# Performance work log

Hardware: AMD Instinct MI355X
Metric: run time of the kernel (lower is better)

Reference implementation:

```python
import jax, jax.numpy as jnp
import numpy as np

EPS = 1e-5

def _layernorm(x, gamma, beta):
    mu = jnp.mean(x, axis=-1, keepdims=True)
    var = jnp.mean(jnp.square(x - mu), axis=-1, keepdims=True)
    return (x - mu) * jax.lax.rsqrt(var + EPS) * gamma + beta

def setup_inputs() -> dict:
    key = jax.random.key(0)
    kx, kw = jax.random.split(key)
    N, D, BIT = 65536, 1024, 64
    X = jax.random.normal(kx, (N, D), dtype=jnp.float32)
    # xavier_uniform with gain=0.5 for weight [BIT, D]
    limit = 0.5 * np.sqrt(6.0 / (D + BIT))
    W = jax.random.uniform(kw, (BIT, D), minval=-limit, maxval=limit, dtype=jnp.float32)
    b = jnp.zeros((BIT,), dtype=jnp.float32)
    ln1_g = jnp.ones((D,), dtype=jnp.float32)
    ln1_b = jnp.zeros((D,), dtype=jnp.float32)
    ln2_g = jnp.ones((BIT,), dtype=jnp.float32)
    ln2_b = jnp.zeros((BIT,), dtype=jnp.float32)
    return {"X": X, "W": W, "b": b, "ln1_g": ln1_g, "ln1_b": ln1_b, "ln2_g": ln2_g, "ln2_b": ln2_b}

def reference(X, W, b, ln1_g, ln1_b, ln2_g, ln2_b):
    # LayerNorm -> Linear -> LayerNorm
    xn = _layernorm(X, ln1_g, ln1_b)                       # [N, D]
    logits = jnp.einsum('nd,bd->nb', xn, W) + b            # [N, BIT]
    logits = _layernorm(logits, ln2_g, ln2_b)
    # mean-center over batch, tanh, sign-binarize
    logits = logits - jnp.mean(logits, axis=0, keepdims=True)
    H = jnp.tanh(0.5 * logits)
    B = jnp.where(H >= 0.0, jnp.int8(1), jnp.int8(-1))
    return H, B
```

## Files before the change

kernel.cpp:

```cpp
#include <hip/hip_runtime.h>
#include <stdint.h>

#define N_ROWS 65536
#define D_IN   1024
#define NBIT   64
#define LN_EPS 1e-5f

typedef __attribute__((ext_vector_type(8)))  _Float16 f16x8;
typedef __attribute__((ext_vector_type(4)))  float f32x4;
typedef __attribute__((ext_vector_type(16))) float f32x16;

__device__ __forceinline__ void gload_lds16(const void* g, void* l) {
    __builtin_amdgcn_global_load_lds(
        (const __attribute__((address_space(1))) uint32_t*)g,
        (__attribute__((address_space(3))) uint32_t*)l, 16, 0, 0);
}

__device__ __forceinline__ f32x16 mfma32(f16x8 a, f16x8 b, f32x16 c) {
    return __builtin_amdgcn_mfma_f32_32x32x16_f16(a, b, c, 0, 0, 0);
}

__global__ void prep_kernel(const float* __restrict__ W, const float* __restrict__ bias,
                            const float* __restrict__ g1, const float* __restrict__ b1,
                            _Float16* __restrict__ whi, _Float16* __restrict__ wlo,
                            float* __restrict__ u, float* __restrict__ v) {
    int bit = blockIdx.x;
    int t   = threadIdx.x;
    int nt  = bit >> 5, col = bit & 31;
    float su = 0.f, sv = 0.f;
    for (int d = t; d < D_IN; d += 256) {
        float w  = W[bit * D_IN + d];
        float gw = w * g1[d];
        su += gw;
        sv += w * b1[d];
        int tg = d >> 4, c = tg >> 3, tt = tg & 7;
        int hi = (d >> 3) & 1, j = d & 7;
        int lane = col + 32 * hi;
        size_t idx = (size_t)c * 8192 + tt * 1024 + nt * 512 + lane * 8 + j;
        _Float16 h = (_Float16)gw;
        whi[idx] = h;
        wlo[idx] = (_Float16)((gw - (float)h) * 2048.0f);
    }
    __shared__ float s1[256], s2[256];
    s1[t] = su; s2[t] = sv;
    __syncthreads();
    for (int off = 128; off > 0; off >>= 1) {
        if (t < off) { s1[t] += s1[t + off]; s2[t] += s2[t + off]; }
        __syncthreads();
    }
    if (t == 0) { u[bit] = s1[0]; v[bit] = s2[0] + bias[bit]; }
}

__global__ void __launch_bounds__(256, 2) main_kernel(
        const float* __restrict__ X,
        const _Float16* __restrict__ whi, const _Float16* __restrict__ wlo,
        const float* __restrict__ u, const float* __restrict__ v,
        const float* __restrict__ g2, const float* __restrict__ b2,
        float* __restrict__ L, float* __restrict__ P) {
    __shared__ _Float16 lw[2][16384];
    int tid  = threadIdx.x;
    int wid  = tid >> 6, lane = tid & 63;
    int col  = lane & 31, hi = lane >> 5;
    int row_base = blockIdx.x * 128 + wid * 32;

    const float* xrow = X + (size_t)(row_base + col) * D_IN + hi * 8;

    const _Float16* gsrc = ((wid & 2) ? wlo : whi) + (wid & 1) * 4096 + (size_t)lane * 8;
    const int ldst = ((wid & 2) ? 8192 : 0) + (wid & 1) * 4096;

#define STAGEW(cc, buf) do {                                                  \
        const _Float16* gs_ = gsrc + (size_t)(cc) * 8192;                     \
        _Float16* ld_ = &lw[buf][ldst];                                       \
        _Pragma("unroll")                                                     \
        for (int r = 0; r < 8; ++r)                                           \
            gload_lds16(gs_ + r * 512, ld_ + r * 512);                        \
    } while (0)

    f32x16 aH0[2], aH1[2], aM[2], aLL[2];
#pragma unroll
    for (int nt = 0; nt < 2; ++nt) {
        aH0[nt] = (f32x16)(0.f); aH1[nt] = (f32x16)(0.f);
        aM[nt]  = (f32x16)(0.f); aLL[nt] = (f32x16)(0.f);
    }
    float sum = 0.f, sumsq = 0.f;

    STAGEW(0, 0);
    __syncthreads();

    for (int c = 0; c < 8; ++c) {
        if (c < 7) STAGEW(c + 1, (c + 1) & 1);
        const float* xp = xrow + c * 128;
        const _Float16* lwb = &lw[c & 1][0] + lane * 8;
#pragma unroll
        for (int t = 0; t < 8; ++t) {
            f32x4 x0 = *(const f32x4*)(xp + t * 16);
            f32x4 x1 = *(const f32x4*)(xp + t * 16 + 4);
            float xs[8] = {x0[0], x0[1], x0[2], x0[3], x1[0], x1[1], x1[2], x1[3]};
            f16x8 ahi, alo;
#pragma unroll
            for (int j = 0; j < 8; ++j) {
                float xv = xs[j];
                sum += xv;
                sumsq = fmaf(xv, xv, sumsq);
                _Float16 h = (_Float16)xv;
                ahi[j] = h;
                alo[j] = (_Float16)((xv - (float)h) * 2048.0f);
            }
            const _Float16* base = lwb + t * 1024;
#pragma unroll
            for (int nt = 0; nt < 2; ++nt) {
                f16x8 bh = *(const f16x8*)(base + nt * 512);
                f16x8 bl = *(const f16x8*)(base + nt * 512 + 8192);
                if (t & 1) aH1[nt] = mfma32(ahi, bh, aH1[nt]);
                else       aH0[nt] = mfma32(ahi, bh, aH0[nt]);
                aM[nt]  = mfma32(ahi, bl, aM[nt]);
                aM[nt]  = mfma32(alo, bh, aM[nt]);
                aLL[nt] = mfma32(alo, bl, aLL[nt]);
            }
        }
        __syncthreads();
    }

    sum   += __shfl_xor(sum, 32);
    sumsq += __shfl_xor(sumsq, 32);
    float mu   = sum * (1.f / 1024.f);
    float var  = sumsq * (1.f / 1024.f) - mu * mu;
    float rstd = rsqrtf(var + LN_EPS);

    float uv[2], vv[2], g2v[2], b2v[2];
#pragma unroll
    for (int nt = 0; nt < 2; ++nt) {
        int bitc = nt * 32 + col;
        uv[nt] = u[bitc]; vv[nt] = v[bitc]; g2v[nt] = g2[bitc]; b2v[nt] = b2[bitc];
    }

    float ps0 = 0.f, ps1 = 0.f;
#pragma unroll
    for (int reg = 0; reg < 16; ++reg) {
        int r = (reg & 3) + 8 * (reg >> 2) + 4 * hi;
        float mu_r = __shfl(mu, r);
        float rs_r = __shfl(rstd, r);
        float lg0, lg1;
        {
            float d0 = (aH0[0][reg] + aH1[0][reg])
                     + aM[0][reg] * (1.0f / 2048.0f)
                     + aLL[0][reg] * (1.0f / 4194304.0f);
            float d1 = (aH0[1][reg] + aH1[1][reg])
                     + aM[1][reg] * (1.0f / 2048.0f)
                     + aLL[1][reg] * (1.0f / 4194304.0f);
            lg0 = rs_r * d0 - rs_r * mu_r * uv[0] + vv[0];
            lg1 = rs_r * d1 - rs_r * mu_r * uv[1] + vv[1];
        }
        float s1 = lg0 + lg1;
        float s2 = lg0 * lg0 + lg1 * lg1;
#pragma unroll
        for (int m = 1; m <= 16; m <<= 1) {
            s1 += __shfl_xor(s1, m);
            s2 += __shfl_xor(s2, m);
        }
        float mean = s1 * (1.f / 64.f);
        float va   = s2 * (1.f / 64.f) - mean * mean;
        float rs2  = rsqrtf(va + LN_EPS);
        float o0 = (lg0 - mean) * rs2 * g2v[0] + b2v[0];
        float o1 = (lg1 - mean) * rs2 * g2v[1] + b2v[1];
        size_t row = (size_t)(row_base + r);
        L[row * 64 + col]      = o0;
        L[row * 64 + 32 + col] = o1;
        ps0 += o0;
        ps1 += o1;
    }

    ps0 += __shfl_xor(ps0, 32);
    ps1 += __shfl_xor(ps1, 32);
    if (hi == 0) {
        P[(size_t)col * 2048        + blockIdx.x * 4 + wid] = ps0;
        P[(size_t)(32 + col) * 2048 + blockIdx.x * 4 + wid] = ps1;
    }
#undef STAGEW
}

__global__ void reduce_kernel(const float* __restrict__ P, float* __restrict__ cm) {
    int bit = blockIdx.x, t = threadIdx.x;
    float s = 0.f;
    for (int p = t; p < 2048; p += 256) s += P[(size_t)bit * 2048 + p];
    __shared__ float sh[256];
    sh[t] = s;
    __syncthreads();
    for (int off = 128; off > 0; off >>= 1) {
        if (t < off) sh[t] += sh[t + off];
        __syncthreads();
    }
    if (t == 0) cm[bit] = sh[0] * (1.f / (float)N_ROWS);
}

__global__ void final_kernel(const float* __restrict__ L, const float* __restrict__ cm,
                             float* __restrict__ out) {
    __shared__ float cms[64];
    if (threadIdx.x < 64) cms[threadIdx.x] = cm[threadIdx.x];
    __syncthreads();
    const f32x4* L4 = (const f32x4*)L;
    f32x4* H4 = (f32x4*)out;
    f32x4* B4 = (f32x4*)(out + (size_t)N_ROWS * NBIT);
    int total = N_ROWS * NBIT / 4;
    for (int i = blockIdx.x * blockDim.x + threadIdx.x; i < total;
         i += gridDim.x * blockDim.x) {
        f32x4 x = L4[i];
        int bb = (i & 15) * 4;
        f32x4 h, bo;
#pragma unroll
        for (int j = 0; j < 4; ++j) {
            float y  = 0.5f * (x[j] - cms[bb + j]);
            float y2 = y * y;
            float poly = y * fmaf(y2, fmaf(y2, 2.f / 15.f, -1.f / 3.f), 1.f);
            float e  = __expf(2.f * y);
            float ef = 1.f - 2.f / (e + 1.f);
            float hv = (fabsf(y) < 0.5f) ? poly : ef;
            h[j]  = hv;
            bo[j] = hv >= 0.f ? 1.f : -1.f;
        }
        __builtin_nontemporal_store(h, &H4[i]);
        __builtin_nontemporal_store(bo, &B4[i]);
    }
}

extern "C" void kernel_launch(void* const* d_in, const int* in_sizes, int n_in,
                              void* d_out, int out_size, void* d_ws, size_t ws_size,
                              hipStream_t stream) {
    (void)in_sizes; (void)n_in; (void)out_size; (void)ws_size;
    const float* X  = (const float*)d_in[0];
    const float* W  = (const float*)d_in[1];
    const float* bb = (const float*)d_in[2];
    const float* g1 = (const float*)d_in[3];
    const float* b1 = (const float*)d_in[4];
    const float* g2 = (const float*)d_in[5];
    const float* b2 = (const float*)d_in[6];

    char* ws = (char*)d_ws;
    _Float16* whi = (_Float16*)ws;
    _Float16* wlo = (_Float16*)(ws + 131072);
    float* u  = (float*)(ws + 262144);
    float* v  = (float*)(ws + 266240);
    float* P  = (float*)(ws + 270336);
    float* cm = (float*)(ws + 270336 + 64 * 2048 * 4);

    float* out = (float*)d_out;
    float* L   = out + (size_t)N_ROWS * NBIT;

    prep_kernel<<<64, 256, 0, stream>>>(W, bb, g1, b1, whi, wlo, u, v);
    main_kernel<<<512, 256, 0, stream>>>(X, whi, wlo, u, v, g2, b2, L, P);
    reduce_kernel<<<64, 256, 0, stream>>>(P, cm);
    final_kernel<<<2048, 256, 0, stream>>>(L, cm, out);
}
```

Baseline: 84.39 us.

## Drop lo*lo MFMA term and use single-buffered 256-wide weight chunks

Removes the alo*blo split-precision MFMA product, which contributes at roughly 2^-22 relative scale, so each k-step issues three MFMAs per tile instead of four. The weight staging changes from double-buffered 128-wide chunks (8 iterations) to one 64KB buffer holding 256-wide chunks (4 iterations). Each next chunk is now loaded only after a barrier, with a second barrier afterwards. This trades the overlap of weight loads with compute for fewer loop iterations and a lower MFMA count, and slightly reduces accuracy.

After: 90.24 us. 6.9% more time.

```diff
diff --git a/kernel.cpp b/kernel.cpp
--- a/kernel.cpp
+++ b/kernel.cpp
@@ -33,10 +33,9 @@
         float gw = w * g1[d];
         su += gw;
         sv += w * b1[d];
-        int tg = d >> 4, c = tg >> 3, tt = tg & 7;
-        int hi = (d >> 3) & 1, j = d & 7;
-        int lane = col + 32 * hi;
-        size_t idx = (size_t)c * 8192 + tt * 1024 + nt * 512 + lane * 8 + j;
+        int c = d >> 8, tt = (d >> 4) & 15, hi8 = (d >> 3) & 1, j = d & 7;
+        int lane = col + 32 * hi8;
+        size_t idx = (size_t)c * 16384 + tt * 1024 + nt * 512 + lane * 8 + j;
         _Float16 h = (_Float16)gw;
         whi[idx] = h;
         wlo[idx] = (_Float16)((gw - (float)h) * 2048.0f);
@@ -57,7 +56,7 @@
         const float* __restrict__ u, const float* __restrict__ v,
         const float* __restrict__ g2, const float* __restrict__ b2,
         float* __restrict__ L, float* __restrict__ P) {
-    __shared__ _Float16 lw[2][16384];
+    __shared__ _Float16 lw[32768];
     int tid  = threadIdx.x;
     int wid  = tid >> 6, lane = tid & 63;
     int col  = lane & 31, hi = lane >> 5;
@@ -65,34 +64,32 @@
 
     const float* xrow = X + (size_t)(row_base + col) * D_IN + hi * 8;
 
-    const _Float16* gsrc = ((wid & 2) ? wlo : whi) + (wid & 1) * 4096 + (size_t)lane * 8;
-    const int ldst = ((wid & 2) ? 8192 : 0) + (wid & 1) * 4096;
-
-#define STAGEW(cc, buf) do {                                                  \
-        const _Float16* gs_ = gsrc + (size_t)(cc) * 8192;                     \
-        _Float16* ld_ = &lw[buf][ldst];                                       \
+    const _Float16* gsrc = ((wid & 2) ? wlo : whi) + (wid & 1) * 8192 + (size_t)lane * 8;
+    const int ldst = ((wid & 2) ? 16384 : 0) + (wid & 1) * 8192;
+
+#define STAGEW(cc) do {                                                       \
+        const _Float16* gs_ = gsrc + (size_t)(cc) * 16384;                    \
+        _Float16* ld_ = &lw[ldst];                                            \
         _Pragma("unroll")                                                     \
-        for (int r = 0; r < 8; ++r)                                           \
+        for (int r = 0; r < 16; ++r)                                          \
             gload_lds16(gs_ + r * 512, ld_ + r * 512);                        \
     } while (0)
 
-    f32x16 aH0[2], aH1[2], aM[2], aLL[2];
+    f32x16 aH0[2], aH1[2], aM[2];
 #pragma unroll
     for (int nt = 0; nt < 2; ++nt) {
-        aH0[nt] = (f32x16)(0.f); aH1[nt] = (f32x16)(0.f);
-        aM[nt]  = (f32x16)(0.f); aLL[nt] = (f32x16)(0.f);
+        aH0[nt] = (f32x16)(0.f); aH1[nt] = (f32x16)(0.f); aM[nt] = (f32x16)(0.f);
     }
     float sum = 0.f, sumsq = 0.f;
 
-    STAGEW(0, 0);
-    __syncthreads();
-
-    for (int c = 0; c < 8; ++c) {
-        if (c < 7) STAGEW(c + 1, (c + 1) & 1);
-        const float* xp = xrow + c * 128;
-        const _Float16* lwb = &lw[c & 1][0] + lane * 8;
-#pragma unroll
-        for (int t = 0; t < 8; ++t) {
+    STAGEW(0);
+    __syncthreads();
+
+    for (int c = 0; c < 4; ++c) {
+        const float* xp = xrow + c * 256;
+        const _Float16* lwb = &lw[0] + lane * 8;
+#pragma unroll
+        for (int t = 0; t < 16; ++t) {
             f32x4 x0 = *(const f32x4*)(xp + t * 16);
             f32x4 x1 = *(const f32x4*)(xp + t * 16 + 4);
             float xs[8] = {x0[0], x0[1], x0[2], x0[3], x1[0], x1[1], x1[2], x1[3]};
@@ -110,15 +107,18 @@
 #pragma unroll
             for (int nt = 0; nt < 2; ++nt) {
                 f16x8 bh = *(const f16x8*)(base + nt * 512);
-                f16x8 bl = *(const f16x8*)(base + nt * 512 + 8192);
+                f16x8 bl = *(const f16x8*)(base + nt * 512 + 16384);
                 if (t & 1) aH1[nt] = mfma32(ahi, bh, aH1[nt]);
                 else       aH0[nt] = mfma32(ahi, bh, aH0[nt]);
-                aM[nt]  = mfma32(ahi, bl, aM[nt]);
-                aM[nt]  = mfma32(alo, bh, aM[nt]);
-                aLL[nt] = mfma32(alo, bl, aLL[nt]);
+                aM[nt] = mfma32(ahi, bl, aM[nt]);
+                aM[nt] = mfma32(alo, bh, aM[nt]);
             }
         }
         __syncthreads();
+        if (c < 3) {
+            STAGEW(c + 1);
+            __syncthreads();
+        }
     }
 
     sum   += __shfl_xor(sum, 32);
@@ -140,17 +140,10 @@
         int r = (reg & 3) + 8 * (reg >> 2) + 4 * hi;
         float mu_r = __shfl(mu, r);
         float rs_r = __shfl(rstd, r);
-        float lg0, lg1;
-        {
-            float d0 = (aH0[0][reg] + aH1[0][reg])
-                     + aM[0][reg] * (1.0f / 2048.0f)
-                     + aLL[0][reg] * (1.0f / 4194304.0f);
-            float d1 = (aH0[1][reg] + aH1[1][reg])
-                     + aM[1][reg] * (1.0f / 2048.0f)
-                     + aLL[1][reg] * (1.0f / 4194304.0f);
-            lg0 = rs_r * d0 - rs_r * mu_r * uv[0] + vv[0];
-            lg1 = rs_r * d1 - rs_r * mu_r * uv[1] + vv[1];
-        }
+        float d0 = (aH0[0][reg] + aH1[0][reg]) + aM[0][reg] * (1.0f / 2048.0f);
+        float d1 = (aH0[1][reg] + aH1[1][reg]) + aM[1][reg] * (1.0f / 2048.0f);
+        float lg0 = rs_r * d0 - rs_r * mu_r * uv[0] + vv[0];
+        float lg1 = rs_r * d1 - rs_r * mu_r * uv[1] + vv[1];
         float s1 = lg0 + lg1;
         float s2 = lg0 * lg0 + lg1 * lg1;
 #pragma unroll
```

## Drop lo*lo MFMA term, prefetch next X chunk, use packed f16 conversion

Applied to the files above, without the earlier changes.

Removes the alo*bl MFMA product and its accumulator, cutting matrix work by a quarter at the cost of a tiny precision loss. The first two X vectors of the next chunk are prefetched before a manual barrier, and that barrier waits on vmcnt(4) rather than a full __syncthreads, so global loads overlap with compute. The hi/lo f16 split now uses packed round-toward-zero conversion (cvt_pkrtz), which changes rounding but keeps the residual exact. The hand-written vmcnt wait adds a correctness risk if the count of outstanding loads does not match.

Measured after the change: 81.30 us. 3.7% less time.

```diff
diff --git a/kernel.cpp b/kernel.cpp
--- a/kernel.cpp
+++ b/kernel.cpp
@@ -7,6 +7,8 @@
 #define LN_EPS 1e-5f
 
 typedef __attribute__((ext_vector_type(8)))  _Float16 f16x8;
+typedef __attribute__((ext_vector_type(4)))  _Float16 f16x4;
+typedef __attribute__((ext_vector_type(2)))  _Float16 f16x2;
 typedef __attribute__((ext_vector_type(4)))  float f32x4;
 typedef __attribute__((ext_vector_type(16))) float f32x16;
 
@@ -18,6 +20,39 @@
 
 __device__ __forceinline__ f32x16 mfma32(f16x8 a, f16x8 b, f32x16 c) {
     return __builtin_amdgcn_mfma_f32_32x32x16_f16(a, b, c, 0, 0, 0);
+}
+
+__device__ __forceinline__ f16x2 pkrtz(float a, float b) {
+    return __builtin_bit_cast(f16x2, __builtin_amdgcn_cvt_pkrtz(a, b));
+}
+
+__device__ __forceinline__ void split8(f32x4 x0, f32x4 x1,
+                                       f16x8& ahi, f16x8& alo,
+                                       float& sum, float& sumsq) {
+    float xs[8] = {x0[0], x0[1], x0[2], x0[3], x1[0], x1[1], x1[2], x1[3]};
+#pragma unroll
+    for (int j = 0; j < 8; ++j) {
+        sum += xs[j];
+        sumsq = fmaf(xs[j], xs[j], sumsq);
+    }
+    f16x2 h01 = pkrtz(xs[0], xs[1]);
+    f16x2 h23 = pkrtz(xs[2], xs[3]);
+    f16x2 h45 = pkrtz(xs[4], xs[5]);
+    f16x2 h67 = pkrtz(xs[6], xs[7]);
+    f16x2 l01 = pkrtz((xs[0] - (float)h01[0]) * 2048.f,
+                      (xs[1] - (float)h01[1]) * 2048.f);
+    f16x2 l23 = pkrtz((xs[2] - (float)h23[0]) * 2048.f,
+                      (xs[3] - (float)h23[1]) * 2048.f);
+    f16x2 l45 = pkrtz((xs[4] - (float)h45[0]) * 2048.f,
+                      (xs[5] - (float)h45[1]) * 2048.f);
+    f16x2 l67 = pkrtz((xs[6] - (float)h67[0]) * 2048.f,
+                      (xs[7] - (float)h67[1]) * 2048.f);
+    f16x4 a0 = __builtin_shufflevector(h01, h23, 0, 1, 2, 3);
+    f16x4 a1 = __builtin_shufflevector(h45, h67, 0, 1, 2, 3);
+    ahi = __builtin_shufflevector(a0, a1, 0, 1, 2, 3, 4, 5, 6, 7);
+    f16x4 b0 = __builtin_shufflevector(l01, l23, 0, 1, 2, 3);
+    f16x4 b1 = __builtin_shufflevector(l45, l67, 0, 1, 2, 3);
+    alo = __builtin_shufflevector(b0, b1, 0, 1, 2, 3, 4, 5, 6, 7);
 }
 
 __global__ void prep_kernel(const float* __restrict__ W, const float* __restrict__ bias,
@@ -34,8 +69,8 @@
         su += gw;
         sv += w * b1[d];
         int tg = d >> 4, c = tg >> 3, tt = tg & 7;
-        int hi = (d >> 3) & 1, j = d & 7;
-        int lane = col + 32 * hi;
+        int hi8 = (d >> 3) & 1, j = d & 7;
+        int lane = col + 32 * hi8;
         size_t idx = (size_t)c * 8192 + tt * 1024 + nt * 512 + lane * 8 + j;
         _Float16 h = (_Float16)gw;
         whi[idx] = h;
@@ -76,36 +111,32 @@
             gload_lds16(gs_ + r * 512, ld_ + r * 512);                        \
     } while (0)
 
-    f32x16 aH0[2], aH1[2], aM[2], aLL[2];
+#define SB0 __builtin_amdgcn_sched_barrier(0)
+
+    f32x16 aH0[2], aH1[2], aM[2];
 #pragma unroll
     for (int nt = 0; nt < 2; ++nt) {
-        aH0[nt] = (f32x16)(0.f); aH1[nt] = (f32x16)(0.f);
-        aM[nt]  = (f32x16)(0.f); aLL[nt] = (f32x16)(0.f);
+        aH0[nt] = (f32x16)(0.f); aH1[nt] = (f32x16)(0.f); aM[nt] = (f32x16)(0.f);
     }
     float sum = 0.f, sumsq = 0.f;
+    f32x4 p0, p1, p2, p3;
 
     STAGEW(0, 0);
+    p0 = *(const f32x4*)(xrow);
+    p1 = *(const f32x4*)(xrow + 4);
+    p2 = *(const f32x4*)(xrow + 16);
+    p3 = *(const f32x4*)(xrow + 20);
     __syncthreads();
 
+#pragma unroll
     for (int c = 0; c < 8; ++c) {
         if (c < 7) STAGEW(c + 1, (c + 1) & 1);
-        const float* xp = xrow + c * 128;
+        const float* xp  = xrow + c * 128;
         const _Float16* lwb = &lw[c & 1][0] + lane * 8;
-#pragma unroll
-        for (int t = 0; t < 8; ++t) {
-            f32x4 x0 = *(const f32x4*)(xp + t * 16);
-            f32x4 x1 = *(const f32x4*)(xp + t * 16 + 4);
-            float xs[8] = {x0[0], x0[1], x0[2], x0[3], x1[0], x1[1], x1[2], x1[3]};
-            f16x8 ahi, alo;
-#pragma unroll
-            for (int j = 0; j < 8; ++j) {
-                float xv = xs[j];
-                sum += xv;
-                sumsq = fmaf(xv, xv, sumsq);
-                _Float16 h = (_Float16)xv;
-                ahi[j] = h;
-                alo[j] = (_Float16)((xv - (float)h) * 2048.0f);
-            }
+        f16x8 ahi, alo;
+#pragma unroll
+        for (int t = 0; t < 2; ++t) {
+            split8(t ? p2 : p0, t ? p3 : p1, ahi, alo, sum, sumsq);
             const _Float16* base = lwb + t * 1024;
 #pragma unroll
             for (int nt = 0; nt < 2; ++nt) {
@@ -113,12 +144,36 @@
                 f16x8 bl = *(const f16x8*)(base + nt * 512 + 8192);
                 if (t & 1) aH1[nt] = mfma32(ahi, bh, aH1[nt]);
                 else       aH0[nt] = mfma32(ahi, bh, aH0[nt]);
-                aM[nt]  = mfma32(ahi, bl, aM[nt]);
-                aM[nt]  = mfma32(alo, bh, aM[nt]);
-                aLL[nt] = mfma32(alo, bl, aLL[nt]);
+                aM[nt] = mfma32(ahi, bl, aM[nt]);
+                aM[nt] = mfma32(alo, bh, aM[nt]);
             }
         }
-        __syncthreads();
+#pragma unroll
+        for (int t = 2; t < 8; ++t) {
+            f32x4 x0 = *(const f32x4*)(xp + t * 16);
+            f32x4 x1 = *(const f32x4*)(xp + t * 16 + 4);
+            split8(x0, x1, ahi, alo, sum, sumsq);
+            const _Float16* base = lwb + t * 1024;
+#pragma unroll
+            for (int nt = 0; nt < 2; ++nt) {
+                f16x8 bh = *(const f16x8*)(base + nt * 512);
+                f16x8 bl = *(const f16x8*)(base + nt * 512 + 8192);
+                if (t & 1) aH1[nt] = mfma32(ahi, bh, aH1[nt]);
+                else       aH0[nt] = mfma32(ahi, bh, aH0[nt]);
+                aM[nt] = mfma32(ahi, bl, aM[nt]);
+                aM[nt] = mfma32(alo, bh, aM[nt]);
+            }
+        }
+        if (c < 7) {
+            const float* xn = xrow + (c + 1) * 128;
+            p0 = *(const f32x4*)(xn);
+            p1 = *(const f32x4*)(xn + 4);
+            p2 = *(const f32x4*)(xn + 16);
+            p3 = *(const f32x4*)(xn + 20);
+            SB0;
+            asm volatile("s_waitcnt vmcnt(4)" ::: "memory");
+            __builtin_amdgcn_s_barrier();
+        }
     }
 
     sum   += __shfl_xor(sum, 32);
@@ -140,17 +195,10 @@
         int r = (reg & 3) + 8 * (reg >> 2) + 4 * hi;
         float mu_r = __shfl(mu, r);
         float rs_r = __shfl(rstd, r);
-        float lg0, lg1;
-        {
-            float d0 = (aH0[0][reg] + aH1[0][reg])
-                     + aM[0][reg] * (1.0f / 2048.0f)
-                     + aLL[0][reg] * (1.0f / 4194304.0f);
-            float d1 = (aH0[1][reg] + aH1[1][reg])
-                     + aM[1][reg] * (1.0f / 2048.0f)
-                     + aLL[1][reg] * (1.0f / 4194304.0f);
-            lg0 = rs_r * d0 - rs_r * mu_r * uv[0] + vv[0];
-            lg1 = rs_r * d1 - rs_r * mu_r * uv[1] + vv[1];
-        }
+        float d0 = (aH0[0][reg] + aH1[0][reg]) + aM[0][reg] * (1.0f / 2048.0f);
+        float d1 = (aH0[1][reg] + aH1[1][reg]) + aM[1][reg] * (1.0f / 2048.0f);
+        float lg0 = rs_r * d0 - rs_r * mu_r * uv[0] + vv[0];
+        float lg1 = rs_r * d1 - rs_r * mu_r * uv[1] + vv[1];
         float s1 = lg0 + lg1;
         float s2 = lg0 * lg0 + lg1 * lg1;
 #pragma unroll
@@ -177,6 +225,7 @@
         P[(size_t)(32 + col) * 2048 + blockIdx.x * 4 + wid] = ps1;
     }
 #undef STAGEW
+#undef SB0
 }
 
 __global__ void reduce_kernel(const float* __restrict__ P, float* __restrict__ cm) {
```
